# Optimization experiments

Hardware: AMD Instinct MI355X
Metric: run time of the kernel (lower is better)

The kernel has to match this reference:

```python
import jax, jax.numpy as jnp
import numpy as np

BS, SL, CL = 32, 512, 20      # batch, seq_len (visits), codes per visit
D, H, V = 256, 4, 20000       # d_model, heads, vocab_size
HD = D // H                   # size_per_head = 64
EPS = 1e-5


def make_pe_table(d_model, max_pos):
    # torch PositionalEncoding: sinusoidal table with a zero pad row prepended
    pe = np.array([[pos / np.power(10000, 2.0 * (j // 2) / d_model)
                    for j in range(d_model)] for pos in range(max_pos)])
    pe[:, 0::2] = np.sin(pe[:, 0::2])
    pe[:, 1::2] = np.cos(pe[:, 1::2])
    pe = np.concatenate([np.zeros((1, d_model)), pe], axis=0)
    return jnp.asarray(pe, dtype=jnp.float32)  # [max_pos+1, d]


def layer_norm(x, g, b):
    mu = jnp.mean(x, axis=-1, keepdims=True)
    var = jnp.mean(jnp.square(x - mu), axis=-1, keepdims=True)
    return (x - mu) * jax.lax.rsqrt(var + EPS) * g + b


def setup_inputs() -> dict:
    key = jax.random.key(0)
    ks = jax.random.split(key, 12)
    input_seqs = jax.random.randint(ks[0], (BS, SL, CL), 0, V, dtype=jnp.int32)
    masks = jnp.ones((BS, SL, SL), dtype=jnp.int32)
    lengths = jax.random.randint(ks[1], (BS,), 1, SL + 1, dtype=jnp.int32)
    seq_time_step = jax.random.uniform(ks[2], (BS, SL), dtype=jnp.float32)
    code_masks = jax.random.uniform(ks[3], (BS, SL, CL), dtype=jnp.float32)

    emb_table = jax.random.normal(ks[4], (V + 1, D), dtype=jnp.float32) * 0.02
    emb_table = emb_table.at[V].set(0.0)  # padding_idx row (never indexed here)
    bound = 1.0 / np.sqrt(V)
    bias_emb = jax.random.uniform(ks[5], (D,), minval=-bound, maxval=bound, dtype=jnp.float32)
    s = 1.0 / np.sqrt(D)
    Wq = jax.random.uniform(ks[6], (D, D), minval=-s, maxval=s, dtype=jnp.float32)
    Wk = jax.random.uniform(ks[7], (D, D), minval=-s, maxval=s, dtype=jnp.float32)
    Wv = jax.random.uniform(ks[8], (D, D), minval=-s, maxval=s, dtype=jnp.float32)
    Wfc = jax.random.uniform(ks[9], (D, D), minval=-s, maxval=s, dtype=jnp.float32)
    ln_g = jnp.ones((D,), dtype=jnp.float32)
    ln_b = jnp.zeros((D,), dtype=jnp.float32)
    so = 1.0 / np.sqrt(4 * D)
    out_w = jax.random.uniform(ks[10], (2, 4 * D), minval=-so, maxval=so, dtype=jnp.float32)
    out_b = jax.random.uniform(ks[11], (2,), minval=-so, maxval=so, dtype=jnp.float32)
    pe_table = make_pe_table(D, SL)

    return dict(input_seqs=input_seqs, masks=masks, lengths=lengths,
                seq_time_step=seq_time_step, code_masks=code_masks,
                emb_table=emb_table, bias_emb=bias_emb, pe_table=pe_table,
                Wq=Wq, Wk=Wk, Wv=Wv, Wfc=Wfc, ln_g=ln_g, ln_b=ln_b,
                out_w=out_w, out_b=out_b)


def reference(input_seqs, masks, lengths, seq_time_step, code_masks,
              emb_table, bias_emb, pe_table, Wq, Wk, Wv, Wfc,
              ln_g, ln_b, out_w, out_b):
    bs, sl, _ = input_seqs.shape
    # visit embedding: sum of code embeddings + bias  -> [bs, sl, d]
    x = emb_table[input_seqs].sum(axis=2) + bias_emb
    # positional encoding: pos ids = 1..len, 0 beyond length
    t_idx = jnp.arange(sl, dtype=jnp.int32)
    pos_ids = jnp.where(t_idx[None, :] < lengths[:, None], t_idx[None, :] + 1, 0)
    x = x + pe_table[pos_ids]
    res = x
    # manual MHA -- NOTE faithful to original: view(bs, H, sl, hd) directly
    q = (x @ Wq.T).reshape(bs, H, sl, HD)
    k = (x @ Wk.T).reshape(bs, H, sl, HD)
    v = (x @ Wv.T).reshape(bs, H, sl, HD)
    energy = jnp.einsum('bhqd,bhkd->bhqk', q, k) / np.sqrt(HD)
    energy = jnp.where(masks[:, None, :, :] == 0, -jnp.inf, energy)
    attn = jax.nn.softmax(energy, axis=-1)
    o = jnp.einsum('bhqk,bhkd->bhqd', attn, v)          # [bs,H,sl,hd]
    o = o.transpose(0, 2, 1, 3).reshape(bs, sl, D)
    x = layer_norm(o @ Wfc.T + res, ln_g, ln_b)
    # zero out positions >= length
    valid = (t_idx[None, :] < lengths[:, None])          # [bs, sl]
    x = jnp.where(valid[:, :, None], x, 0.0)
    # triangular-weighted temporal pooling into 4 bins (vectorized loops)
    lens = lengths.astype(jnp.float32)
    t = jnp.arange(1, sl + 1, dtype=jnp.float32)
    s_val = 4.0 * t[None, :] / lens[:, None]             # [bs, sl]
    m = jnp.arange(1, 5, dtype=jnp.float32)              # 4 bins
    w = jnp.square(1.0 - jnp.abs(s_val[:, :, None] - m[None, None, :]) / 4.0)  # [bs,sl,4]
    U = jnp.einsum('bsm,bsd->bmd', w, x)                 # [bs,4,d]
    U = U.reshape(bs, 4 * D)
    return U @ out_w.T + out_b                           # [bs, 2]
```

## Files before the change

kernel.cpp:

```cpp
#include <hip/hip_runtime.h>

#define BSZ 32
#define SLEN 512
#define CLEN 20
#define DMOD 256
#define NH 4
#define HDIM 64

typedef _Float16 half8 __attribute__((ext_vector_type(8)));
typedef _Float16 half4 __attribute__((ext_vector_type(4)));
typedef float float4v __attribute__((ext_vector_type(4)));

#define MFMA16(a, b, c) __builtin_amdgcn_mfma_f32_16x16x32_f16(a, b, c, 0, 0, 0)
#define PG(fi) ((((fi) >> 4) * 17) + ((fi) & 15))

__global__ __launch_bounds__(256) void k_cast(
    const float* __restrict__ W0, const float* __restrict__ W1,
    const float* __restrict__ W2, const float* __restrict__ W3,
    const float* __restrict__ emb,
    _Float16* __restrict__ wh, _Float16* __restrict__ embh) {
  const int bid = blockIdx.x;
  const float* src;
  _Float16* dst;
  int idx;
  if (bid < 128) {
    const int z = bid >> 5;
    src = (z == 0) ? W0 : (z == 1) ? W1 : (z == 2) ? W2 : W3;
    dst = wh + (size_t)z * 65536;
    idx = ((bid & 31) * 256 + threadIdx.x) * 8;
  } else {
    src = emb;
    dst = embh;
    idx = ((bid - 128) * 256 + threadIdx.x) * 8;
  }
  float v[8];
  *(float4*)v = *(const float4*)(src + idx);
  *(float4*)(v + 4) = *(const float4*)(src + idx + 4);
  half8 h;
  #pragma unroll
  for (int i = 0; i < 8; ++i) h[i] = (_Float16)v[i];
  *(half8*)(dst + idx) = h;
}

__global__ __launch_bounds__(256) void k_embmask(
    const int* __restrict__ seqs, const int* __restrict__ lengths,
    const _Float16* __restrict__ embh, const float* __restrict__ bias,
    const float* __restrict__ pe, _Float16* __restrict__ x,
    const int* __restrict__ masks, unsigned int* __restrict__ pk) {
  const int row0 = blockIdx.x * 8;
  const int sub = threadIdx.x >> 5;
  const int hl = threadIdx.x & 31;
  const int row = row0 + sub;
  const int b = row >> 9, s = row & 511;
  __shared__ int codes[8][CLEN];
  if (threadIdx.x < 8 * CLEN)
    codes[threadIdx.x / CLEN][threadIdx.x % CLEN] = seqs[row0 * CLEN + threadIdx.x];
  __syncthreads();
  const int pos = (s < lengths[b]) ? (s + 1) : 0;
  const int d = hl * 8;
  float acc[8];
  *(float4*)acc = *(const float4*)(bias + d);
  *(float4*)(acc + 4) = *(const float4*)(bias + d + 4);
  const float4 pv0 = *(const float4*)(pe + (size_t)pos * DMOD + d);
  const float4 pv1 = *(const float4*)(pe + (size_t)pos * DMOD + d + 4);
  acc[0] += pv0.x; acc[1] += pv0.y; acc[2] += pv0.z; acc[3] += pv0.w;
  acc[4] += pv1.x; acc[5] += pv1.y; acc[6] += pv1.z; acc[7] += pv1.w;
  #pragma unroll
  for (int c = 0; c < CLEN; ++c) {
    const half8 ev = *(const half8*)(embh + (size_t)codes[sub][c] * DMOD + d);
    #pragma unroll
    for (int i = 0; i < 8; ++i) acc[i] += (float)ev[i];
  }
  half8 hv;
  #pragma unroll
  for (int i = 0; i < 8; ++i) hv[i] = (_Float16)acc[i];
  *(half8*)(x + (size_t)row * DMOD + d) = hv;
  const int wv = threadIdx.x >> 6;
  const int lane = threadIdx.x & 63;
  #pragma unroll
  for (int p = 0; p < 16; ++p) {
    const int it = wv + p * 4;
    const int r = row0 + (it >> 3);
    const int chunk = it & 7;
    const int m = masks[(size_t)r * SLEN + chunk * 64 + lane];
    const unsigned long long bal = __ballot(m != 0);
    if (lane == 0) {
      pk[(size_t)r * 16 + chunk * 2]     = (unsigned int)bal;
      pk[(size_t)r * 16 + chunk * 2 + 1] = (unsigned int)(bal >> 32);
    }
  }
}

__global__ __launch_bounds__(256) void k_gemm_qkv(
    const _Float16* __restrict__ A, const _Float16* __restrict__ Wb,
    _Float16* __restrict__ q, _Float16* __restrict__ k, _Float16* __restrict__ v) {
  const int z = blockIdx.z;
  _Float16* Cb = (z == 0) ? q : (z == 1) ? k : v;
  const _Float16* w_ = Wb + (size_t)z * 65536;
  const int m0 = blockIdx.x * 128;
  const int n0 = blockIdx.y * 128;
  const int tid = threadIdx.x;
  const int lane = tid & 63;
  const int w = tid >> 6;
  const int wm = (w >> 1) * 4;
  const int wn = (w & 1) * 4;
  __shared__ _Float16 smem[8704];
  half8* As = (half8*)(smem);
  half8* Ws = (half8*)(smem + 4096);
  float4v acc[4][4];
  #pragma unroll
  for (int i = 0; i < 4; ++i)
    #pragma unroll
    for (int j = 0; j < 4; ++j)
      acc[i][j] = (float4v){0.f, 0.f, 0.f, 0.f};
  int li_[2]; size_t ga_[2], gw_[2];
  #pragma unroll
  for (int p = 0; p < 2; ++p) {
    const int c = tid + p * 256;
    const int r = c & 127, qd = c >> 7;
    li_[p] = (r >> 4) * 64 + qd * 16 + (r & 15);
    ga_[p] = (size_t)(m0 + r) * DMOD + qd * 8;
    gw_[p] = (size_t)(n0 + r) * DMOD + qd * 8;
  }
  half8 pa[2], pw[2];
  #pragma unroll
  for (int p = 0; p < 2; ++p) {
    pa[p] = *(const half8*)(A + ga_[p]);
    pw[p] = *(const half8*)(w_ + gw_[p]);
  }
  for (int k0 = 0; k0 < DMOD; k0 += 32) {
    #pragma unroll
    for (int p = 0; p < 2; ++p) {
      As[li_[p]] = pa[p];
      Ws[li_[p]] = pw[p];
    }
    __syncthreads();
    if (k0 + 32 < DMOD) {
      #pragma unroll
      for (int p = 0; p < 2; ++p) {
        pa[p] = *(const half8*)(A + ga_[p] + k0 + 32);
        pw[p] = *(const half8*)(w_ + gw_[p] + k0 + 32);
      }
    }
    half8 af[4], wf[4];
    #pragma unroll
    for (int i = 0; i < 4; ++i) {
      af[i] = As[(wm + i) * 64 + lane];
      wf[i] = Ws[(wn + i) * 64 + lane];
    }
    #pragma unroll
    for (int i = 0; i < 4; ++i)
      #pragma unroll
      for (int j = 0; j < 4; ++j)
        acc[i][j] = MFMA16(af[i], wf[j], acc[i][j]);
    __syncthreads();
  }
  const int cr = (lane >> 4) * 4;
  const int cc = lane & 15;
  _Float16* Eh = smem;
  #pragma unroll
  for (int ip = 0; ip < 4; ++ip) {
    #pragma unroll
    for (int j = 0; j < 4; ++j) {
      const int col = (wn + j) * 16 + cc;
      #pragma unroll
      for (int r = 0; r < 4; ++r)
        Eh[((w >> 1) * 16 + cr + r) * 136 + col] = (_Float16)acc[ip][j][r];
    }
    __syncthreads();
    #pragma unroll
    for (int e = 0; e < 2; ++e) {
      const int idx = tid + e * 256;
      const int lr = idx >> 4;
      const int cg = idx & 15;
      const int gr = m0 + (lr >> 4) * 64 + ip * 16 + (lr & 15);
      *(half8*)(Cb + (size_t)gr * DMOD + n0 + cg * 8) =
          *(const half8*)&Eh[lr * 136 + cg * 8];
    }
    __syncthreads();
  }
}

__global__ __launch_bounds__(256) void k_vt(
    const _Float16* __restrict__ v, _Float16* __restrict__ vt) {
  const int bh = blockIdx.x;
  const size_t off = (size_t)bh * 32768;
  __shared__ _Float16 Th[64][66];
  const int tid = threadIdx.x;
  const int sc = blockIdx.y * 64;
  #pragma unroll
  for (int p = 0; p < 2; ++p) {
    const int lin = tid + p * 256;
    const int r = lin >> 3, g = lin & 7;
    *(half8*)&Th[r][g * 8] = *(const half8*)(v + off + (size_t)(sc + r) * 64 + g * 8);
  }
  __syncthreads();
  #pragma unroll
  for (int p = 0; p < 2; ++p) {
    const int lin = tid + p * 256;
    const int d = lin >> 3, sg = lin & 7;
    half8 hv;
    #pragma unroll
    for (int j = 0; j < 8; ++j) hv[j] = Th[sg * 8 + j][d];
    *(half8*)(vt + off + (size_t)d * 512 + sc + sg * 8) = hv;
  }
}

__global__ __launch_bounds__(256) void k_gemm_fc(
    const _Float16* __restrict__ A, const _Float16* __restrict__ w_,
    float* __restrict__ C, const _Float16* __restrict__ res) {
  const int m0 = blockIdx.x * 128;
  const int n0 = blockIdx.y * 128;
  const int tid = threadIdx.x;
  const int lane = tid & 63;
  const int w = tid >> 6;
  const int wm = (w >> 1) * 4;
  const int wn = (w & 1) * 4;
  __shared__ half8 As[512], Ws[512];
  float4v acc[4][4];
  #pragma unroll
  for (int i = 0; i < 4; ++i)
    #pragma unroll
    for (int j = 0; j < 4; ++j)
      acc[i][j] = (float4v){0.f, 0.f, 0.f, 0.f};
  int li_[2]; size_t ga_[2], gw_[2];
  #pragma unroll
  for (int p = 0; p < 2; ++p) {
    const int c = tid + p * 256;
    const int r = c & 127, qd = c >> 7;
    li_[p] = (r >> 4) * 64 + qd * 16 + (r & 15);
    ga_[p] = (size_t)(m0 + r) * DMOD + qd * 8;
    gw_[p] = (size_t)(n0 + r) * DMOD + qd * 8;
  }
  half8 pa[2], pw[2];
  #pragma unroll
  for (int p = 0; p < 2; ++p) {
    pa[p] = *(const half8*)(A + ga_[p]);
    pw[p] = *(const half8*)(w_ + gw_[p]);
  }
  for (int k0 = 0; k0 < DMOD; k0 += 32) {
    #pragma unroll
    for (int p = 0; p < 2; ++p) {
      As[li_[p]] = pa[p];
      Ws[li_[p]] = pw[p];
    }
    __syncthreads();
    if (k0 + 32 < DMOD) {
      #pragma unroll
      for (int p = 0; p < 2; ++p) {
        pa[p] = *(const half8*)(A + ga_[p] + k0 + 32);
        pw[p] = *(const half8*)(w_ + gw_[p] + k0 + 32);
      }
    }
    half8 af[4], wf[4];
    #pragma unroll
    for (int i = 0; i < 4; ++i) {
      af[i] = As[(wm + i) * 64 + lane];
      wf[i] = Ws[(wn + i) * 64 + lane];
    }
    #pragma unroll
    for (int i = 0; i < 4; ++i)
      #pragma unroll
      for (int j = 0; j < 4; ++j)
        acc[i][j] = MFMA16(af[i], wf[j], acc[i][j]);
    __syncthreads();
  }
  const int cr = (lane >> 4) * 4;
  const int cc = lane & 15;
  #pragma unroll
  for (int i = 0; i < 4; ++i) {
    const int gm = m0 + (wm + i) * 16 + cr;
    #pragma unroll
    for (int j = 0; j < 4; ++j) {
      const int gc = n0 + (wn + j) * 16 + cc;
      #pragma unroll
      for (int r = 0; r < 4; ++r) {
        const size_t flat = (size_t)(gm + r) * DMOD + gc;
        C[flat] = acc[i][j][r] + (float)res[flat];
      }
    }
  }
}

__global__ __launch_bounds__(256, 2) void k_attn(
    const _Float16* __restrict__ q_, const _Float16* __restrict__ k_,
    const _Float16* __restrict__ vt, const unsigned int* __restrict__ pk,
    _Float16* __restrict__ o) {
  const int L = blockIdx.x;
  const int bh = (L & 7) * 16 + ((L >> 3) & 15);
  const int q0 = (L >> 7) * 128;
  const size_t bhoff = (size_t)bh * 32768;
  __shared__ half8 QP[1088];
  __shared__ half8 Ks[544], Vs[544];
  __shared__ unsigned long long Ms64[128];
  __shared__ float Ps[4][128];
  __shared__ float lsum[128];
  const int tid = threadIdx.x;
  const int w = tid >> 6;
  const int lane = tid & 63;
  const int l15 = lane & 15;
  const int quad = lane >> 4;
  #pragma unroll
  for (int p = 0; p < 4; ++p) {
    const int lin = tid + p * 256;
    const int r = lin >> 3, g = lin & 7;
    const int fi = (r >> 4) * 128 + g * 16 + (r & 15);
    QP[PG(fi)] = *(const half8*)(q_ + bhoff + (size_t)(q0 + r) * 64 + g * 8);
  }
  __syncthreads();
  half8 qf[8][2];
  #pragma unroll
  for (int ns = 0; ns < 8; ++ns) {
    const int gq = ns * 8 + quad;
    qf[ns][0] = QP[gq * 17 + l15];
    qf[ns][1] = QP[(gq + 4) * 17 + l15];
  }
  float4v oacc[8];
  float lsw[8] = {0.f, 0.f, 0.f, 0.f, 0.f, 0.f, 0.f, 0.f};
  #pragma unroll
  for (int ns = 0; ns < 8; ++ns) oacc[ns] = (float4v){0.f, 0.f, 0.f, 0.f};
  for (int kc = 0; kc < SLEN; kc += 64) {
    __syncthreads();
    #pragma unroll
    for (int p = 0; p < 2; ++p) {
      const int lin = tid + p * 256;
      const int r = lin >> 3, g = lin & 7;
      const int fi = PG((r >> 4) * 128 + g * 16 + (r & 15));
      Ks[fi] = *(const half8*)(k_ + bhoff + (size_t)(kc + r) * 64 + g * 8);
      Vs[fi] = *(const half8*)(vt + bhoff + (size_t)r * 512 + kc + g * 8);
    }
    ((unsigned int*)Ms64)[tid] =
        pk[((size_t)((bh >> 2) << 9) + q0 + (tid >> 1)) * 16 + (kc >> 5) + (tid & 1)];
    __syncthreads();
    const int ga0 = (w * 8 + quad) * 17 + l15;
    const int ga1 = (w * 8 + quad + 4) * 17 + l15;
    const half8 ah0 = Ks[ga0], ah1 = Ks[ga1];
    #pragma unroll
    for (int ns = 0; ns < 8; ++ns) {
      float4v s = (float4v){0.f, 0.f, 0.f, 0.f};
      s = MFMA16(ah0, qf[ns][0], s);
      s = MFMA16(ah1, qf[ns][1], s);
      const int q = ns * 16 + l15;
      const unsigned long long mrow = Ms64[q];
      const unsigned mbits = (unsigned)(mrow >> (w * 16 + quad * 4)) & 15u;
      half4 h4;
      #pragma unroll
      for (int r = 0; r < 4; ++r) {
        const float pe = ((mbits >> r) & 1u) ? __expf(s[r] * 0.125f) : 0.f;
        h4[r] = (_Float16)pe;
        lsw[ns] += pe;
      }
      const int hb = ((ns * 8 + w * 2 + (quad >> 1)) * 17 + l15) * 8 + (quad & 1) * 4;
      *(half4*)((_Float16*)QP + hb) = h4;
    }
    __syncthreads();
    const half8 vh0 = Vs[ga0], vh1 = Vs[ga1];
    #pragma unroll
    for (int ns = 0; ns < 8; ++ns) {
      const int pb0 = (ns * 8 + quad) * 17 + l15;
      const int pb1 = (ns * 8 + quad + 4) * 17 + l15;
      oacc[ns] = MFMA16(vh0, QP[pb0], oacc[ns]);
      oacc[ns] = MFMA16(vh1, QP[pb1], oacc[ns]);
    }
  }
  #pragma unroll
  for (int ns = 0; ns < 8; ++ns) {
    lsw[ns] += __shfl_xor(lsw[ns], 16);
    lsw[ns] += __shfl_xor(lsw[ns], 32);
  }
  __syncthreads();
  if (quad == 0) {
    #pragma unroll
    for (int ns = 0; ns < 8; ++ns) Ps[w][ns * 16 + l15] = lsw[ns];
  }
  __syncthreads();
  if (tid < 128) lsum[tid] = Ps[0][tid] + Ps[1][tid] + Ps[2][tid] + Ps[3][tid];
  __syncthreads();
  const int b = bh >> 2, h = bh & 3;
  _Float16* Ot = (_Float16*)QP;
  #pragma unroll
  for (int ns = 0; ns < 8; ++ns) {
    const int q = ns * 16 + l15;
    const float inv = 1.0f / lsum[q];
    half4 h4;
    #pragma unroll
    for (int r = 0; r < 4; ++r) h4[r] = (_Float16)(oacc[ns][r] * inv);
    *(half4*)&Ot[q * 68 + w * 16 + quad * 4] = h4;
  }
  __syncthreads();
  #pragma unroll
  for (int e = 0; e < 4; ++e) {
    const int idx = tid + e * 256;
    const int qq = idx >> 3, g = idx & 7;
    *(half8*)(o + ((size_t)(b * SLEN + q0 + qq)) * DMOD + h * HDIM + g * 8) =
        *(const half8*)&Ot[qq * 68 + g * 8];
  }
}

__global__ __launch_bounds__(256) void k_lnpool(
    const float* __restrict__ Y, const int* __restrict__ lengths,
    const float* __restrict__ g, const float* __restrict__ bb,
    float* __restrict__ Up) {
  const int b = blockIdx.x;
  const int c = blockIdx.y;
  const int tid = threadIdx.x;
  const int w = tid >> 6;
  const int lane = tid & 63;
  __shared__ float Pl[4][4][DMOD];
  const int len = lengths[b];
  const float inv4 = 4.0f / (float)len;
  float gg[4], bv[4];
  *(float4*)gg = *(const float4*)(g + lane * 4);
  *(float4*)bv = *(const float4*)(bb + lane * 4);
  float a[4][4] = {};
  for (int t = 0; t < 8; ++t) {
    const int r = c * 32 + t * 4 + w;
    float v[4];
    *(float4*)v = *(const float4*)(Y + ((size_t)b * SLEN + r) * DMOD + lane * 4);
    float sum = v[0] + v[1] + v[2] + v[3];
    float sq = v[0] * v[0] + v[1] * v[1] + v[2] * v[2] + v[3] * v[3];
    #pragma unroll
    for (int off = 32; off > 0; off >>= 1) {
      sum += __shfl_xor(sum, off);
      sq += __shfl_xor(sq, off);
    }
    const float mu = sum * (1.0f / DMOD);
    const float inv = rsqrtf(sq * (1.0f / DMOD) - mu * mu + 1e-5f);
    const bool valid = r < len;
    float ov[4];
    #pragma unroll
    for (int i = 0; i < 4; ++i)
      ov[i] = valid ? ((v[i] - mu) * inv * gg[i] + bv[i]) : 0.f;
    const float sv = (float)(r + 1) * inv4;
    #pragma unroll
    for (int m = 0; m < 4; ++m) {
      const float tm = 1.0f - fabsf(sv - (float)(m + 1)) * 0.25f;
      const float t2 = tm * tm;
      #pragma unroll
      for (int i = 0; i < 4; ++i) a[m][i] += t2 * ov[i];
    }
  }
  #pragma unroll
  for (int m = 0; m < 4; ++m)
    *(float4*)&Pl[w][m][lane * 4] = *(float4*)a[m];
  __syncthreads();
  #pragma unroll
  for (int e = 0; e < 4; ++e) {
    const int idx = tid + e * 256;
    const int m = idx >> 8, d = idx & 255;
    const float s = Pl[0][m][d] + Pl[1][m][d] + Pl[2][m][d] + Pl[3][m][d];
    Up[(((size_t)b * 16 + c) * 4 + m) * DMOD + d] = s;
  }
}

__global__ __launch_bounds__(256) void k_out(
    const float* __restrict__ Up, const float* __restrict__ ow,
    const float* __restrict__ ob, float* __restrict__ out) {
  const int b = blockIdx.x;
  const int tid = threadIdx.x;
  const int w = tid >> 6;
  const int lane = tid & 63;
  __shared__ float rr[8];
  float4 s = {0.f, 0.f, 0.f, 0.f};
  #pragma unroll
  for (int c = 0; c < 16; ++c) {
    const float4 u = *(const float4*)(Up + ((size_t)b * 16 + c) * 1024 + tid * 4);
    s.x += u.x; s.y += u.y; s.z += u.z; s.w += u.w;
  }
  const float4 w0 = *(const float4*)(ow + tid * 4);
  const float4 w1 = *(const float4*)(ow + 1024 + tid * 4);
  float acc0 = s.x * w0.x + s.y * w0.y + s.z * w0.z + s.w * w0.w;
  float acc1 = s.x * w1.x + s.y * w1.y + s.z * w1.z + s.w * w1.w;
  #pragma unroll
  for (int off = 32; off > 0; off >>= 1) {
    acc0 += __shfl_xor(acc0, off);
    acc1 += __shfl_xor(acc1, off);
  }
  if (lane == 0) { rr[w] = acc0; rr[4 + w] = acc1; }
  __syncthreads();
  if (tid == 0) {
    out[b * 2 + 0] = rr[0] + rr[1] + rr[2] + rr[3] + ob[0];
    out[b * 2 + 1] = rr[4] + rr[5] + rr[6] + rr[7] + ob[1];
  }
}

extern "C" void kernel_launch(void* const* d_in, const int* in_sizes, int n_in,
                              void* d_out, int out_size, void* d_ws, size_t ws_size,
                              hipStream_t stream) {
  const int* seqs     = (const int*)d_in[0];
  const int* masks    = (const int*)d_in[1];
  const int* lengths  = (const int*)d_in[2];
  const float* emb    = (const float*)d_in[5];
  const float* bias   = (const float*)d_in[6];
  const float* pe     = (const float*)d_in[7];
  const float* Wq     = (const float*)d_in[8];
  const float* Wk     = (const float*)d_in[9];
  const float* Wv     = (const float*)d_in[10];
  const float* Wfc    = (const float*)d_in[11];
  const float* ln_g   = (const float*)d_in[12];
  const float* ln_b   = (const float*)d_in[13];
  const float* out_w  = (const float*)d_in[14];
  const float* out_b  = (const float*)d_in[15];
  float* outp = (float*)d_out;

  const size_t NE = (size_t)BSZ * SLEN * DMOD;
  _Float16* q = (_Float16*)d_ws;
  _Float16* k = q + NE;
  _Float16* v = k + NE;
  _Float16* vt = v + NE;
  _Float16* x = vt + NE;
  _Float16* o = x + NE;
  _Float16* wh = o + NE;
  unsigned int* pk = (unsigned int*)(wh + 4 * 65536);
  float* Up = (float*)(pk + BSZ * SLEN * 16);
  float* y = (float*)q;
  _Float16* embh = (_Float16*)d_ws;

  k_cast<<<2628, 256, 0, stream>>>(Wq, Wk, Wv, Wfc, emb, wh, embh);
  k_embmask<<<BSZ * SLEN / 8, 256, 0, stream>>>(seqs, lengths, embh, bias, pe, x,
                                                masks, pk);
  k_gemm_qkv<<<dim3(128, 2, 3), 256, 0, stream>>>(x, wh, q, k, v);
  k_vt<<<dim3(BSZ * NH, 8), 256, 0, stream>>>(v, vt);
  k_attn<<<BSZ * NH * (SLEN / 128), 256, 0, stream>>>(q, k, vt, pk, o);
  k_gemm_fc<<<dim3(128, 2), 256, 0, stream>>>(o, wh + 3 * 65536, y, x);
  k_lnpool<<<dim3(BSZ, 16), 256, 0, stream>>>(y, lengths, ln_g, ln_b, Up);
  k_out<<<BSZ, 256, 0, stream>>>(Up, out_w, out_b, outp);
}
```

Measured before the change: 222.4 us.

## Fuse FC GEMM with residual, LayerNorm and temporal pooling epilogue

Merges the output-projection GEMM and the LayerNorm+pooling kernel into one kernel. Each block now computes a full 64-row by 256-column tile, so the row statistics and the pooled partial sums come straight from registers. This removes the fp32 intermediate write and read of Y and one kernel launch. In exchange the grid drops from 256 blocks of 128x128 tiles to 256 blocks of 64x256 tiles, each block loads the full weight matrix per k-step, and the epilogue adds shuffle and shared-memory reductions.

```diff
diff --git a/kernel.cpp b/kernel.cpp
--- a/kernel.cpp
+++ b/kernel.cpp
@@ -206,57 +206,56 @@
   }
 }
 
-__global__ __launch_bounds__(256) void k_gemm_fc(
+__global__ __launch_bounds__(256) void k_fcln(
     const _Float16* __restrict__ A, const _Float16* __restrict__ w_,
-    float* __restrict__ C, const _Float16* __restrict__ res) {
-  const int m0 = blockIdx.x * 128;
-  const int n0 = blockIdx.y * 128;
+    const _Float16* __restrict__ res, const int* __restrict__ lengths,
+    const float* __restrict__ g, const float* __restrict__ bb,
+    float* __restrict__ Up) {
+  const int m0 = blockIdx.x * 64;
+  const int b = m0 >> 9;
+  const int s0 = m0 & 511;
   const int tid = threadIdx.x;
   const int lane = tid & 63;
   const int w = tid >> 6;
-  const int wm = (w >> 1) * 4;
-  const int wn = (w & 1) * 4;
-  __shared__ half8 As[512], Ws[512];
+  __shared__ half8 As[256], Ws[1024];
+  __shared__ float Rs[4][64], Rq[4][64];
+  __shared__ float Fmu[64], Fiv[64];
   float4v acc[4][4];
   #pragma unroll
   for (int i = 0; i < 4; ++i)
     #pragma unroll
     for (int j = 0; j < 4; ++j)
       acc[i][j] = (float4v){0.f, 0.f, 0.f, 0.f};
-  int li_[2]; size_t ga_[2], gw_[2];
-  #pragma unroll
-  for (int p = 0; p < 2; ++p) {
+  const int ra = tid & 63, qa = tid >> 6;
+  const int li_a = (ra >> 4) * 64 + qa * 16 + (ra & 15);
+  const size_t ga_ = (size_t)(m0 + ra) * DMOD + qa * 8;
+  int li_w[4]; size_t gw_[4];
+  #pragma unroll
+  for (int p = 0; p < 4; ++p) {
     const int c = tid + p * 256;
-    const int r = c & 127, qd = c >> 7;
-    li_[p] = (r >> 4) * 64 + qd * 16 + (r & 15);
-    ga_[p] = (size_t)(m0 + r) * DMOD + qd * 8;
-    gw_[p] = (size_t)(n0 + r) * DMOD + qd * 8;
-  }
-  half8 pa[2], pw[2];
-  #pragma unroll
-  for (int p = 0; p < 2; ++p) {
-    pa[p] = *(const half8*)(A + ga_[p]);
-    pw[p] = *(const half8*)(w_ + gw_[p]);
-  }
+    const int rw = c & 255, qw = c >> 8;
+    li_w[p] = (rw >> 4) * 64 + qw * 16 + (rw & 15);
+    gw_[p] = (size_t)rw * DMOD + qw * 8;
+  }
+  half8 pa = *(const half8*)(A + ga_);
+  half8 pw[4];
+  #pragma unroll
+  for (int p = 0; p < 4; ++p) pw[p] = *(const half8*)(w_ + gw_[p]);
   for (int k0 = 0; k0 < DMOD; k0 += 32) {
-    #pragma unroll
-    for (int p = 0; p < 2; ++p) {
-      As[li_[p]] = pa[p];
-      Ws[li_[p]] = pw[p];
-    }
+    As[li_a] = pa;
+    #pragma unroll
+    for (int p = 0; p < 4; ++p) Ws[li_w[p]] = pw[p];
     __syncthreads();
     if (k0 + 32 < DMOD) {
-      #pragma unroll
-      for (int p = 0; p < 2; ++p) {
-        pa[p] = *(const half8*)(A + ga_[p] + k0 + 32);
-        pw[p] = *(const half8*)(w_ + gw_[p] + k0 + 32);
-      }
+      pa = *(const half8*)(A + ga_ + k0 + 32);
+      #pragma unroll
+      for (int p = 0; p < 4; ++p) pw[p] = *(const half8*)(w_ + gw_[p] + k0 + 32);
     }
     half8 af[4], wf[4];
     #pragma unroll
     for (int i = 0; i < 4; ++i) {
-      af[i] = As[(wm + i) * 64 + lane];
-      wf[i] = Ws[(wn + i) * 64 + lane];
+      af[i] = As[i * 64 + lane];
+      wf[i] = Ws[(w * 4 + i) * 64 + lane];
     }
     #pragma unroll
     for (int i = 0; i < 4; ++i)
@@ -267,18 +266,98 @@
   }
   const int cr = (lane >> 4) * 4;
   const int cc = lane & 15;
-  #pragma unroll
-  for (int i = 0; i < 4; ++i) {
-    const int gm = m0 + (wm + i) * 16 + cr;
+  const int l15 = cc;
+  #pragma unroll
+  for (int i = 0; i < 4; ++i)
     #pragma unroll
     for (int j = 0; j < 4; ++j) {
-      const int gc = n0 + (wn + j) * 16 + cc;
+      const int col = (w * 4 + j) * 16 + cc;
+      #pragma unroll
+      for (int r = 0; r < 4; ++r)
+        acc[i][j][r] += (float)res[(size_t)(m0 + i * 16 + cr + r) * DMOD + col];
+    }
+  float S[4][4], Q2[4][4];
+  #pragma unroll
+  for (int i = 0; i < 4; ++i)
+    #pragma unroll
+    for (int r = 0; r < 4; ++r) {
+      float s = 0.f, q2 = 0.f;
+      #pragma unroll
+      for (int j = 0; j < 4; ++j) {
+        const float v = acc[i][j][r];
+        s += v; q2 += v * v;
+      }
+      #pragma unroll
+      for (int off = 1; off <= 8; off <<= 1) {
+        s += __shfl_xor(s, off);
+        q2 += __shfl_xor(q2, off);
+      }
+      S[i][r] = s; Q2[i][r] = q2;
+    }
+  if (l15 == 0) {
+    #pragma unroll
+    for (int i = 0; i < 4; ++i)
       #pragma unroll
       for (int r = 0; r < 4; ++r) {
-        const size_t flat = (size_t)(gm + r) * DMOD + gc;
-        C[flat] = acc[i][j][r] + (float)res[flat];
-      }
-    }
+        Rs[w][i * 16 + cr + r] = S[i][r];
+        Rq[w][i * 16 + cr + r] = Q2[i][r];
+      }
+  }
+  __syncthreads();
+  if (tid < 64) {
+    const float s = Rs[0][tid] + Rs[1][tid] + Rs[2][tid] + Rs[3][tid];
+    const float q2 = Rq[0][tid] + Rq[1][tid] + Rq[2][tid] + Rq[3][tid];
+    const float mu = s * (1.0f / DMOD);
+    Fmu[tid] = mu;
+    Fiv[tid] = rsqrtf(q2 * (1.0f / DMOD) - mu * mu + 1e-5f);
+  }
+  __syncthreads();
+  const int len = lengths[b];
+  const float inv4 = 4.0f / (float)len;
+  float gl[4], bl[4];
+  #pragma unroll
+  for (int j = 0; j < 4; ++j) {
+    const int col = (w * 4 + j) * 16 + cc;
+    gl[j] = g[col]; bl[j] = bb[col];
+  }
+  float pool[4][4] = {};
+  #pragma unroll
+  for (int i = 0; i < 4; ++i)
+    #pragma unroll
+    for (int r = 0; r < 4; ++r) {
+      const int row_l = i * 16 + cr + r;
+      const int sg = s0 + row_l;
+      const bool valid = sg < len;
+      const float mu = Fmu[row_l], iv = Fiv[row_l];
+      const float sv = (float)(sg + 1) * inv4;
+      float t2[4];
+      #pragma unroll
+      for (int m = 0; m < 4; ++m) {
+        const float tm = 1.0f - fabsf(sv - (float)(m + 1)) * 0.25f;
+        t2[m] = tm * tm;
+      }
+      #pragma unroll
+      for (int j = 0; j < 4; ++j) {
+        const float ov = valid ? (acc[i][j][r] - mu) * iv * gl[j] + bl[j] : 0.f;
+        #pragma unroll
+        for (int m = 0; m < 4; ++m) pool[m][j] += t2[m] * ov;
+      }
+    }
+  #pragma unroll
+  for (int m = 0; m < 4; ++m)
+    #pragma unroll
+    for (int j = 0; j < 4; ++j) {
+      pool[m][j] += __shfl_xor(pool[m][j], 16);
+      pool[m][j] += __shfl_xor(pool[m][j], 32);
+    }
+  const int sc = (m0 >> 6) & 7;
+  if ((lane >> 4) == 0) {
+    #pragma unroll
+    for (int m = 0; m < 4; ++m)
+      #pragma unroll
+      for (int j = 0; j < 4; ++j)
+        Up[(((size_t)b * 8 + sc) * 4 + m) * DMOD + (w * 4 + j) * 16 + cc] =
+            pool[m][j];
   }
 }
 
@@ -397,62 +476,6 @@
   }
 }
 
-__global__ __launch_bounds__(256) void k_lnpool(
-    const float* __restrict__ Y, const int* __restrict__ lengths,
-    const float* __restrict__ g, const float* __restrict__ bb,
-    float* __restrict__ Up) {
-  const int b = blockIdx.x;
-  const int c = blockIdx.y;
-  const int tid = threadIdx.x;
-  const int w = tid >> 6;
-  const int lane = tid & 63;
-  __shared__ float Pl[4][4][DMOD];
-  const int len = lengths[b];
-  const float inv4 = 4.0f / (float)len;
-  float gg[4], bv[4];
-  *(float4*)gg = *(const float4*)(g + lane * 4);
-  *(float4*)bv = *(const float4*)(bb + lane * 4);
-  float a[4][4] = {};
-  for (int t = 0; t < 8; ++t) {
-    const int r = c * 32 + t * 4 + w;
-    float v[4];
-    *(float4*)v = *(const float4*)(Y + ((size_t)b * SLEN + r) * DMOD + lane * 4);
-    float sum = v[0] + v[1] + v[2] + v[3];
-    float sq = v[0] * v[0] + v[1] * v[1] + v[2] * v[2] + v[3] * v[3];
-    #pragma unroll
-    for (int off = 32; off > 0; off >>= 1) {
-      sum += __shfl_xor(sum, off);
-      sq += __shfl_xor(sq, off);
-    }
-    const float mu = sum * (1.0f / DMOD);
-    const float inv = rsqrtf(sq * (1.0f / DMOD) - mu * mu + 1e-5f);
-    const bool valid = r < len;
-    float ov[4];
-    #pragma unroll
-    for (int i = 0; i < 4; ++i)
-      ov[i] = valid ? ((v[i] - mu) * inv * gg[i] + bv[i]) : 0.f;
-    const float sv = (float)(r + 1) * inv4;
-    #pragma unroll
-    for (int m = 0; m < 4; ++m) {
-      const float tm = 1.0f - fabsf(sv - (float)(m + 1)) * 0.25f;
-      const float t2 = tm * tm;
-      #pragma unroll
-      for (int i = 0; i < 4; ++i) a[m][i] += t2 * ov[i];
-    }
-  }
-  #pragma unroll
-  for (int m = 0; m < 4; ++m)
-    *(float4*)&Pl[w][m][lane * 4] = *(float4*)a[m];
-  __syncthreads();
-  #pragma unroll
-  for (int e = 0; e < 4; ++e) {
-    const int idx = tid + e * 256;
-    const int m = idx >> 8, d = idx & 255;
-    const float s = Pl[0][m][d] + Pl[1][m][d] + Pl[2][m][d] + Pl[3][m][d];
-    Up[(((size_t)b * 16 + c) * 4 + m) * DMOD + d] = s;
-  }
-}
-
 __global__ __launch_bounds__(256) void k_out(
     const float* __restrict__ Up, const float* __restrict__ ow,
     const float* __restrict__ ob, float* __restrict__ out) {
@@ -463,8 +486,8 @@
   __shared__ float rr[8];
   float4 s = {0.f, 0.f, 0.f, 0.f};
   #pragma unroll
-  for (int c = 0; c < 16; ++c) {
-    const float4 u = *(const float4*)(Up + ((size_t)b * 16 + c) * 1024 + tid * 4);
+  for (int c = 0; c < 8; ++c) {
+    const float4 u = *(const float4*)(Up + ((size_t)b * 8 + c) * 1024 + tid * 4);
     s.x += u.x; s.y += u.y; s.z += u.z; s.w += u.w;
   }
   const float4 w0 = *(const float4*)(ow + tid * 4);
@@ -513,7 +536,6 @@
   _Float16* wh = o + NE;
   unsigned int* pk = (unsigned int*)(wh + 4 * 65536);
   float* Up = (float*)(pk + BSZ * SLEN * 16);
-  float* y = (float*)q;
   _Float16* embh = (_Float16*)d_ws;
 
   k_cast<<<2628, 256, 0, stream>>>(Wq, Wk, Wv, Wfc, emb, wh, embh);
@@ -522,7 +544,6 @@
   k_gemm_qkv<<<dim3(128, 2, 3), 256, 0, stream>>>(x, wh, q, k, v);
   k_vt<<<dim3(BSZ * NH, 8), 256, 0, stream>>>(v, vt);
   k_attn<<<BSZ * NH * (SLEN / 128), 256, 0, stream>>>(q, k, vt, pk, o);
-  k_gemm_fc<<<dim3(128, 2), 256, 0, stream>>>(o, wh + 3 * 65536, y, x);
-  k_lnpool<<<dim3(BSZ, 16), 256, 0, stream>>>(y, lengths, ln_g, ln_b, Up);
+  k_fcln<<<256, 256, 0, stream>>>(o, wh + 3 * 65536, x, lengths, ln_g, ln_b, Up);
   k_out<<<BSZ, 256, 0, stream>>>(Up, out_w, out_b, outp);
 }
```

After: 217.5 us. -2.2%, faster.
